# Kernel optimization log

Hardware: AMD Instinct MI355X
Metric: run time of the kernel (lower is better)

Reference implementation:

```python
import jax, jax.numpy as jnp
import numpy as np
from jax import lax

DIVISOR = 2.0


def setup_inputs() -> dict:
    key = jax.random.key(0)
    k1, k2, k3, k4 = jax.random.split(key, 4)
    x = jax.random.normal(k1, (128, 8, 32, 32, 32), dtype=jnp.float32)
    conv_weight = jax.random.normal(k2, (16, 8, 3, 3, 3), dtype=jnp.float32) * 0.1
    conv_bias = jax.random.normal(k3, (16,), dtype=jnp.float32) * 0.1
    bias = jax.random.normal(k4, (16, 1, 1, 1), dtype=jnp.float32) * 0.1
    return {"x": x, "conv_weight": conv_weight, "conv_bias": conv_bias, "bias": bias}


def reference(x, conv_weight, conv_bias, bias):
    # Conv3d, stride 1, no padding: [B,8,32,32,32] -> [B,16,30,30,30]
    y = lax.conv_general_dilated(
        x, conv_weight,
        window_strides=(1, 1, 1), padding='VALID',
        dimension_numbers=('NCDHW', 'OIDHW', 'NCDHW'))
    y = y + conv_bias[None, :, None, None, None]
    # divide by scalar divisor
    y = y / DIVISOR
    # MaxPool3d kernel=stride=2: [B,16,30,30,30] -> [B,16,15,15,15]
    y = lax.reduce_window(
        y, -jnp.inf, lax.max,
        window_dimensions=(1, 1, 2, 2, 2),
        window_strides=(1, 1, 2, 2, 2),
        padding='VALID')
    # AdaptiveAvgPool3d((1,1,1)): global mean over D,H,W -> [B,16,1,1,1]
    y = jnp.mean(y, axis=(2, 3, 4), keepdims=True)
    # bias add (bias shape [16,1,1,1] broadcasts over batch)
    y = y + bias
    # sum over channel dim (dim=1) -> [B,1,1,1]
    return jnp.sum(y, axis=1)
```

## Files before the change

### kernel.cpp

```cpp
#include <hip/hip_runtime.h>


using short8 = __attribute__((ext_vector_type(8))) short;
using f32x4  = __attribute__((ext_vector_type(4))) float;

__device__ __forceinline__ unsigned short f2bf(float f) {
  unsigned u = __float_as_uint(f);
  return (unsigned short)((u + 0x7FFFu + ((u >> 16) & 1u)) >> 16);
}

__global__ __launch_bounds__(256) void prep_w(const float* __restrict__ cw,
                                              short* __restrict__ Bp) {
  int i = threadIdx.x + blockIdx.x * 256;
  if (i >= 576) return;
  int g = i >> 6, l = i & 63;
  int co = l & 15, kw = l >> 4;
  int kd = g / 3, kh = g % 3;
  short8 o;
#pragma unroll
  for (int j = 0; j < 8; ++j) {
    float v = (kw < 3) ? cw[(co * 8 + j) * 27 + kd * 9 + kh * 3 + kw] : 0.0f;
    o[j] = (short)f2bf(v);
  }
  *(short8*)(Bp + (size_t)i * 8) = o;
}

__global__ __launch_bounds__(256, 4) void conv_mfma(const float* __restrict__ x,
                                                    const short* __restrict__ Bp,
                                                    float* __restrict__ partial) {
  __shared__ __align__(16) char lds[4 * 18 * 512];
  __shared__ float red[4];

  const int flat = blockIdx.x;
  const int xcd = flat & 7, idx = flat >> 3;
  const int b   = xcd * 16 + idx / 30;
  const int r30 = idx % 30;
  const int pd  = r30 >> 1, hh = r30 & 1;
  const int t = threadIdx.x, lane = t & 63, wv = t >> 6;
  const int d0  = pd * 2;
  const int hbs = hh ? 14 : 0;
  const float* xb = x + (size_t)b * 262144;

  for (int s = t; s < 576; s += 256) {
    const int d = s / 144, rem = s % 144;
    const int hr = rem >> 3, wc = rem & 7;
    const float* gp = xb + (d0 + d) * 1024 + (hbs + hr) * 32 + wc * 4;
    float4 va[8];
#pragma unroll
    for (int ci = 0; ci < 8; ++ci) va[ci] = *(const float4*)(gp + ci * 32768);
    char* rowp = lds + (d * 18 + hr) * 512;
#pragma unroll
    for (int wi = 0; wi < 4; ++wi) {
      const int w = wc * 4 + wi;
      short8 o;
#pragma unroll
      for (int ci = 0; ci < 8; ++ci) o[ci] = (short)f2bf(((const float*)&va[ci])[wi]);
      *(short8*)(rowp + ((w * 16) ^ (((w >> 3) & 3) << 4))) = o;
    }
  }

  short8 Bw[9];
#pragma unroll
  for (int g = 0; g < 9; ++g)
    Bw[g] = *(const short8*)(Bp + ((size_t)g * 64 + lane) * 8);

  const int m = lane & 15, tg = lane >> 4;
  const int w0 = m + tg;
  int w1 = m + 16 + tg; if (w1 > 31) w1 = 31;
  const int wb0 = (w0 * 16) ^ (((w0 >> 3) & 3) << 4);
  const int wb1 = (w1 * 16) ^ (((w1 >> 3) & 3) << 4);

  __syncthreads();

  const int ntasks = hh ? 14 : 16;
  const int rowoff = hh ? 2 : 0;
  float sum = 0.0f;
  for (int tid = wv; tid < ntasks; tid += 4) {
    const int ql = tid >> 1, c = tid & 1;
    const int base = (c ? wb1 : wb0) + (2 * ql + rowoff) * 512;
    f32x4 cc[2][2] = {};
#pragma unroll
    for (int p = 0; p < 4; ++p) {
#pragma unroll
      for (int rr = 0; rr < 4; ++rr) {
        const short8 a = *(const short8*)(lds + base + p * 9216 + rr * 512);
        if (p < 3 && rr < 3)
          cc[0][0] = __builtin_amdgcn_mfma_f32_16x16x32_bf16(a, Bw[p * 3 + rr], cc[0][0], 0, 0, 0);
        if (p < 3 && rr > 0)
          cc[0][1] = __builtin_amdgcn_mfma_f32_16x16x32_bf16(a, Bw[p * 3 + rr - 1], cc[0][1], 0, 0, 0);
        if (p > 0 && rr < 3)
          cc[1][0] = __builtin_amdgcn_mfma_f32_16x16x32_bf16(a, Bw[(p - 1) * 3 + rr], cc[1][0], 0, 0, 0);
        if (p > 0 && rr > 0)
          cc[1][1] = __builtin_amdgcn_mfma_f32_16x16x32_bf16(a, Bw[(p - 1) * 3 + rr - 1], cc[1][1], 0, 0, 0);
      }
    }
#pragma unroll
    for (int p2 = 0; p2 < 2; ++p2) {
      float v = fmaxf(fmaxf(fmaxf(cc[0][0][2 * p2], cc[0][0][2 * p2 + 1]),
                            fmaxf(cc[0][1][2 * p2], cc[0][1][2 * p2 + 1])),
                      fmaxf(fmaxf(cc[1][0][2 * p2], cc[1][0][2 * p2 + 1]),
                            fmaxf(cc[1][1][2 * p2], cc[1][1][2 * p2 + 1])));
      const bool inval = (c == 1) && (tg == 3) && (p2 == 1);
      sum += inval ? 0.0f : v;
    }
  }

#pragma unroll
  for (int off = 32; off; off >>= 1) sum += __shfl_down(sum, off);
  if (lane == 0) red[wv] = sum;
  __syncthreads();
  if (t == 0)
    partial[b * 30 + pd * 2 + hh] = red[0] + red[1] + red[2] + red[3];
}

__global__ __launch_bounds__(64) void finalize(const float* __restrict__ partial,
                                               const float* __restrict__ cb,
                                               const float* __restrict__ bias,
                                               float* __restrict__ out) {
  const int b = blockIdx.x, t = threadIdx.x;
  float s = (t < 30) ? partial[b * 30 + t] : 0.0f;
#pragma unroll
  for (int off = 32; off; off >>= 1) s += __shfl_down(s, off);
  if (t == 0) {
    float k = 0.0f;
#pragma unroll
    for (int c = 0; c < 16; ++c) k += cb[c] * 0.5f + bias[c];
    out[b] = s * (1.0f / 6750.0f) + k;
  }
}

extern "C" void kernel_launch(void* const* d_in, const int* in_sizes, int n_in,
                              void* d_out, int out_size, void* d_ws, size_t ws_size,
                              hipStream_t stream) {
  const float* x    = (const float*)d_in[0];
  const float* cw   = (const float*)d_in[1];
  const float* cb   = (const float*)d_in[2];
  const float* bias = (const float*)d_in[3];
  float* out = (float*)d_out;

  short* Bp      = (short*)d_ws;
  float* partial = (float*)((char*)d_ws + 32768);

  prep_w<<<3, 256, 0, stream>>>(cw, Bp);
  conv_mfma<<<3840, 256, 0, stream>>>(x, Bp, partial);
  finalize<<<128, 64, 0, stream>>>(partial, cb, bias, out);
}
```

Baseline: 46.61 us.

## Stream depth slabs through a ring buffer with prefetch instead of 4-plane halos

Each block now owns a strip of 4 output-pool rows across the whole depth of one batch element and walks the depth dimension. It prefetches the next two input depth planes into registers while MFMA runs on the current four planes held in a 6-slab LDS ring. This removes the depth-halo reloads of the old 2-plane-per-block tiling. Grid size drops from 3840 to 1024 blocks, and the bf16 conversion switches to truncation via v_perm instead of round-to-nearest. The cost is lower parallelism, a barrier per depth step, idle waves in the last strip, and slightly different rounding.

```diff
diff --git a/kernel.cpp b/kernel.cpp
--- a/kernel.cpp
+++ b/kernel.cpp
@@ -4,7 +4,7 @@
 using short8 = __attribute__((ext_vector_type(8))) short;
 using f32x4  = __attribute__((ext_vector_type(4))) float;
 
-__device__ __forceinline__ unsigned short f2bf(float f) {
+__device__ __forceinline__ unsigned short f2bf_rn(float f) {
   unsigned u = __float_as_uint(f);
   return (unsigned short)((u + 0x7FFFu + ((u >> 16) & 1u)) >> 16);
 }
@@ -20,7 +20,7 @@
 #pragma unroll
   for (int j = 0; j < 8; ++j) {
     float v = (kw < 3) ? cw[(co * 8 + j) * 27 + kd * 9 + kh * 3 + kw] : 0.0f;
-    o[j] = (short)f2bf(v);
+    o[j] = (short)f2bf_rn(v);
   }
   *(short8*)(Bp + (size_t)i * 8) = o;
 }
@@ -28,36 +28,50 @@
 __global__ __launch_bounds__(256, 4) void conv_mfma(const float* __restrict__ x,
                                                     const short* __restrict__ Bp,
                                                     float* __restrict__ partial) {
-  __shared__ __align__(16) char lds[4 * 18 * 512];
+  __shared__ __align__(16) char lds[6 * 3072];
   __shared__ float red[4];
 
-  const int flat = blockIdx.x;
-  const int xcd = flat & 7, idx = flat >> 3;
-  const int b   = xcd * 16 + idx / 30;
-  const int r30 = idx % 30;
-  const int pd  = r30 >> 1, hh = r30 & 1;
+  const int bid = blockIdx.x;
+  const int swz = (bid & 7) * 128 + (bid >> 3);
+  const int b = swz >> 3, q = swz & 7;
   const int t = threadIdx.x, lane = t & 63, wv = t >> 6;
-  const int d0  = pd * 2;
-  const int hbs = hh ? 14 : 0;
+  const int nrows = (q == 7) ? 4 : 6;
+  const int row0 = 4 * q;
+  const int nsite = 2 * nrows * 16;
   const float* xb = x + (size_t)b * 262144;
 
-  for (int s = t; s < 576; s += 256) {
-    const int d = s / 144, rem = s % 144;
-    const int hr = rem >> 3, wc = rem & 7;
-    const float* gp = xb + (d0 + d) * 1024 + (hbs + hr) * 32 + wc * 4;
-    float4 va[8];
+  const bool sact = t < nsite;
+  const int ss = sact ? t : 0;
+  const int spl = ss / (nrows * 16);
+  const int rem = ss - spl * (nrows * 16);
+  const int sr = rem >> 4, swg = rem & 15;
+  const float* gsite = xb + (row0 + sr) * 32 + swg * 2;
+
+  auto issue = [&](int dpair, float2* v) {
+    if (!sact) return;
+    const float* gp = gsite + (dpair + spl) * 1024;
 #pragma unroll
-    for (int ci = 0; ci < 8; ++ci) va[ci] = *(const float4*)(gp + ci * 32768);
-    char* rowp = lds + (d * 18 + hr) * 512;
+    for (int ci = 0; ci < 8; ++ci) v[ci] = *(const float2*)(gp + ci * 32768);
+  };
+  auto writeSlab = [&](int dpair, const float2* v) {
+    if (!sact) return;
+    const int d = dpair + spl;
+    char* sb = lds + (d % 6) * 3072 + sr * 512;
 #pragma unroll
-    for (int wi = 0; wi < 4; ++wi) {
-      const int w = wc * 4 + wi;
-      short8 o;
-#pragma unroll
-      for (int ci = 0; ci < 8; ++ci) o[ci] = (short)f2bf(((const float*)&va[ci])[wi]);
-      *(short8*)(rowp + ((w * 16) ^ (((w >> 3) & 3) << 4))) = o;
+    for (int wi = 0; wi < 2; ++wi) {
+      const int w = swg * 2 + wi;
+      uint4 o;
+      o.x = __builtin_amdgcn_perm(__float_as_uint(((const float*)&v[1])[wi]),
+                                  __float_as_uint(((const float*)&v[0])[wi]), 0x07060302u);
+      o.y = __builtin_amdgcn_perm(__float_as_uint(((const float*)&v[3])[wi]),
+                                  __float_as_uint(((const float*)&v[2])[wi]), 0x07060302u);
+      o.z = __builtin_amdgcn_perm(__float_as_uint(((const float*)&v[5])[wi]),
+                                  __float_as_uint(((const float*)&v[4])[wi]), 0x07060302u);
+      o.w = __builtin_amdgcn_perm(__float_as_uint(((const float*)&v[7])[wi]),
+                                  __float_as_uint(((const float*)&v[6])[wi]), 0x07060302u);
+      *(uint4*)(sb + ((w * 16) ^ (((w >> 3) & 3) << 4))) = o;
     }
-  }
+  };
 
   short8 Bw[9];
 #pragma unroll
@@ -70,63 +84,80 @@
   const int wb0 = (w0 * 16) ^ (((w0 >> 3) & 3) << 4);
   const int wb1 = (w1 * 16) ^ (((w1 >> 3) & 3) << 4);
 
+  const bool docomp = (q < 7) || (wv < 2);
+  const int op = (q < 7) ? (wv >> 1) : 0;
+  const int c  = (q < 7) ? (wv & 1) : wv;
+  const int wbase = (c ? wb1 : wb0) + (2 * op) * 512;
+
+  {
+    float2 va[8], vb[8];
+    issue(0, va); issue(2, vb);
+    writeSlab(0, va); writeSlab(2, vb);
+  }
   __syncthreads();
 
-  const int ntasks = hh ? 14 : 16;
-  const int rowoff = hh ? 2 : 0;
   float sum = 0.0f;
-  for (int tid = wv; tid < ntasks; tid += 4) {
-    const int ql = tid >> 1, c = tid & 1;
-    const int base = (c ? wb1 : wb0) + (2 * ql + rowoff) * 512;
-    f32x4 cc[2][2] = {};
+  for (int pd = 0; pd < 15; ++pd) {
+    const bool more = (pd < 14);
+    float2 va[8];
+    if (more) issue(2 * pd + 4, va);
+
+    if (docomp) {
+      const char* sb0 = lds + ((2 * pd)     % 6) * 3072 + wbase;
+      const char* sb1 = lds + ((2 * pd + 1) % 6) * 3072 + wbase;
+      const char* sb2 = lds + ((2 * pd + 2) % 6) * 3072 + wbase;
+      const char* sb3 = lds + ((2 * pd + 3) % 6) * 3072 + wbase;
+      const char* sbp[4] = {sb0, sb1, sb2, sb3};
+      f32x4 cc[2][2] = {};
 #pragma unroll
-    for (int p = 0; p < 4; ++p) {
+      for (int p = 0; p < 4; ++p) {
 #pragma unroll
-      for (int rr = 0; rr < 4; ++rr) {
-        const short8 a = *(const short8*)(lds + base + p * 9216 + rr * 512);
-        if (p < 3 && rr < 3)
-          cc[0][0] = __builtin_amdgcn_mfma_f32_16x16x32_bf16(a, Bw[p * 3 + rr], cc[0][0], 0, 0, 0);
-        if (p < 3 && rr > 0)
-          cc[0][1] = __builtin_amdgcn_mfma_f32_16x16x32_bf16(a, Bw[p * 3 + rr - 1], cc[0][1], 0, 0, 0);
-        if (p > 0 && rr < 3)
-          cc[1][0] = __builtin_amdgcn_mfma_f32_16x16x32_bf16(a, Bw[(p - 1) * 3 + rr], cc[1][0], 0, 0, 0);
-        if (p > 0 && rr > 0)
-          cc[1][1] = __builtin_amdgcn_mfma_f32_16x16x32_bf16(a, Bw[(p - 1) * 3 + rr - 1], cc[1][1], 0, 0, 0);
+        for (int rr = 0; rr < 4; ++rr) {
+          const short8 a = *(const short8*)(sbp[p] + rr * 512);
+          if (p < 3 && rr < 3)
+            cc[0][0] = __builtin_amdgcn_mfma_f32_16x16x32_bf16(a, Bw[p * 3 + rr], cc[0][0], 0, 0, 0);
+          if (p < 3 && rr > 0)
+            cc[0][1] = __builtin_amdgcn_mfma_f32_16x16x32_bf16(a, Bw[p * 3 + rr - 1], cc[0][1], 0, 0, 0);
+          if (p > 0 && rr < 3)
+            cc[1][0] = __builtin_amdgcn_mfma_f32_16x16x32_bf16(a, Bw[(p - 1) * 3 + rr], cc[1][0], 0, 0, 0);
+          if (p > 0 && rr > 0)
+            cc[1][1] = __builtin_amdgcn_mfma_f32_16x16x32_bf16(a, Bw[(p - 1) * 3 + rr - 1], cc[1][1], 0, 0, 0);
+        }
+      }
+#pragma unroll
+      for (int p2 = 0; p2 < 2; ++p2) {
+        float v = fmaxf(fmaxf(fmaxf(cc[0][0][2 * p2], cc[0][0][2 * p2 + 1]),
+                              fmaxf(cc[0][1][2 * p2], cc[0][1][2 * p2 + 1])),
+                        fmaxf(fmaxf(cc[1][0][2 * p2], cc[1][0][2 * p2 + 1]),
+                              fmaxf(cc[1][1][2 * p2], cc[1][1][2 * p2 + 1])));
+        const bool inval = (c == 1) && (tg == 3) && (p2 == 1);
+        sum += inval ? 0.0f : v;
       }
     }
-#pragma unroll
-    for (int p2 = 0; p2 < 2; ++p2) {
-      float v = fmaxf(fmaxf(fmaxf(cc[0][0][2 * p2], cc[0][0][2 * p2 + 1]),
-                            fmaxf(cc[0][1][2 * p2], cc[0][1][2 * p2 + 1])),
-                      fmaxf(fmaxf(cc[1][0][2 * p2], cc[1][0][2 * p2 + 1]),
-                            fmaxf(cc[1][1][2 * p2], cc[1][1][2 * p2 + 1])));
-      const bool inval = (c == 1) && (tg == 3) && (p2 == 1);
-      sum += inval ? 0.0f : v;
-    }
+
+    if (more) writeSlab(2 * pd + 4, va);
+    __syncthreads();
   }
 
 #pragma unroll
   for (int off = 32; off; off >>= 1) sum += __shfl_down(sum, off);
   if (lane == 0) red[wv] = sum;
   __syncthreads();
-  if (t == 0)
-    partial[b * 30 + pd * 2 + hh] = red[0] + red[1] + red[2] + red[3];
+  if (t == 0) partial[b * 8 + q] = red[0] + red[1] + red[2] + red[3];
 }
 
-__global__ __launch_bounds__(64) void finalize(const float* __restrict__ partial,
-                                               const float* __restrict__ cb,
-                                               const float* __restrict__ bias,
-                                               float* __restrict__ out) {
-  const int b = blockIdx.x, t = threadIdx.x;
-  float s = (t < 30) ? partial[b * 30 + t] : 0.0f;
+__global__ __launch_bounds__(128) void finalize(const float* __restrict__ partial,
+                                                const float* __restrict__ cb,
+                                                const float* __restrict__ bias,
+                                                float* __restrict__ out) {
+  const int b = threadIdx.x;
+  float k = 0.0f;
 #pragma unroll
-  for (int off = 32; off; off >>= 1) s += __shfl_down(s, off);
-  if (t == 0) {
-    float k = 0.0f;
+  for (int c = 0; c < 16; ++c) k += cb[c] * 0.5f + bias[c];
+  float s = 0.0f;
 #pragma unroll
-    for (int c = 0; c < 16; ++c) k += cb[c] * 0.5f + bias[c];
-    out[b] = s * (1.0f / 6750.0f) + k;
-  }
+  for (int q = 0; q < 8; ++q) s += partial[b * 8 + q];
+  out[b] = s * (1.0f / 6750.0f) + k;
 }
 
 extern "C" void kernel_launch(void* const* d_in, const int* in_sizes, int n_in,
@@ -142,6 +173,6 @@
   float* partial = (float*)((char*)d_ws + 32768);
 
   prep_w<<<3, 256, 0, stream>>>(cw, Bp);
-  conv_mfma<<<3840, 256, 0, stream>>>(x, Bp, partial);
-  finalize<<<128, 64, 0, stream>>>(partial, cb, bias, out);
+  conv_mfma<<<1024, 256, 0, stream>>>(x, Bp, partial);
+  finalize<<<1, 128, 0, stream>>>(partial, cb, bias, out);
 }
```

New measurement: 42.33 us, median of 2. 1.1x faster.
